# Performance work log

Measured on AMD Instinct MI355X. Metric: run time of the kernel, lower is better.

## Reference

```python
import jax, jax.numpy as jnp
import numpy as np
import itertools

B, NM, NS, K, HID, NLAYER, MAXZ, OUT = 64, 32, 32, 3, 64, 4, 100, 1
S = B * NS
NREAL = NM - 2  # real nodes per graph (rest padded)


def setup_inputs() -> dict:
    key = jax.random.key(0)
    ks = jax.random.split(key, 12)
    x = jax.random.randint(ks[0], (B, NM, 1), 0, MAXZ + 1, dtype=jnp.int32)
    subadj = jax.random.uniform(ks[1], (B, NM, NM), dtype=jnp.float32)
    # K distinct node ids per subgraph, all within the real (non-padded) nodes
    subgs = jnp.argsort(jax.random.uniform(ks[2], (S, NREAL)), axis=1)[:, :K].astype(jnp.int32)
    num_node = jnp.full((B,), NREAL, dtype=jnp.int32)
    num_subg = jnp.full((B,), NS, dtype=jnp.int32)
    sc = 0.05
    idemb = jax.random.normal(ks[3], (K + 2, HID), jnp.float32) * sc
    node_emb = jax.random.normal(ks[4], (MAXZ + 1, HID), jnp.float32) * sc
    mlp_W1 = jax.random.normal(ks[5], (NLAYER, HID, HID), jnp.float32) * sc
    mlp_b1 = jnp.zeros((NLAYER, HID), jnp.float32)
    mlp_W2 = jax.random.normal(ks[6], (NLAYER, HID, HID), jnp.float32) * sc
    mlp_b2 = jnp.zeros((NLAYER, HID), jnp.float32)
    mlp_g = jnp.ones((NLAYER, HID), jnp.float32)
    mlp_be = jnp.zeros((NLAYER, HID), jnp.float32)
    set1_W = jax.random.normal(ks[7], (HID, HID), jnp.float32) * sc
    set1_b = jnp.zeros((HID,), jnp.float32)
    set2_W = jax.random.normal(ks[8], (HID, HID), jnp.float32) * sc
    set2_b = jnp.zeros((HID,), jnp.float32)
    out_W = jax.random.normal(ks[9], (HID, OUT), jnp.float32) * sc
    out_b = jnp.zeros((OUT,), jnp.float32)
    return dict(x=x, subadj=subadj, subgs=subgs, num_node=num_node, num_subg=num_subg,
                idemb=idemb, node_emb=node_emb, mlp_W1=mlp_W1, mlp_b1=mlp_b1,
                mlp_W2=mlp_W2, mlp_b2=mlp_b2, mlp_g=mlp_g, mlp_be=mlp_be,
                set1_W=set1_W, set1_b=set1_b, set2_W=set2_W, set2_b=set2_b,
                out_W=out_W, out_b=out_b)


def _layernorm(z, g, b):
    m = z.mean(-1, keepdims=True)
    v = ((z - m) ** 2).mean(-1, keepdims=True)
    return (z - m) / jnp.sqrt(v + 1e-5) * g + b


def _forward(x, subadj, subgs, num_node,
             idemb, node_emb, mlp_W1, mlp_b1, mlp_W2, mlp_b2, mlp_g, mlp_be,
             set1_W, set1_b, set2_W, set2_b, out_W, out_b):
    # allperm: (K, K!) -- matches registered buffer extracttuple(arange(k),k).t()
    allperm = jnp.asarray(np.array(list(itertools.permutations(range(K))), dtype=np.int32).T)
    P = allperm.shape[1]  # K! permutations
    subgbatch = jnp.repeat(jnp.arange(B), NS)                       # (S,) graph id of each subgraph
    null_mask = jnp.arange(NM)[None, :] >= num_node[:, None]        # (B, NM) padded-node mask
    h = node_emb[x[..., 0]]                                         # (B, NM, HID) inmlp embedding
    h = jnp.broadcast_to(h[subgbatch][:, :, None, :], (S, NM, P, HID))  # gather per subgraph, expand perms
    # CSR scatter-assign of permutation id embeddings (all rows full size K, distinct nodes)
    labelbatch = jnp.repeat(jnp.arange(S), K)                       # (S*K,)
    labelnodes = subgs.reshape(-1)                                  # (S*K,)
    nodeidx = jnp.tile(jnp.arange(K), S)                            # position within subgraph
    emb = idemb[allperm[nodeidx]]                                   # (S*K, P, HID)
    h = h.at[labelbatch, labelnodes].multiply(emb)                  # unique (subg,node) pairs
    A = subadj[subgbatch]                                           # (S, NM, NM), float path (d=1 broadcast)
    for l in range(NLAYER):
        m = jnp.einsum('bij,bjpd->bipd', A, h)                      # noindexbmm
        m = jax.nn.relu(m @ mlp_W1[l] + mlp_b1[l])
        m = m @ mlp_W2[l] + mlp_b2[l]
        m = jax.nn.relu(_layernorm(m, mlp_g[l], mlp_be[l]))
        h = h + m
    h = jnp.where(null_mask[subgbatch][:, :, None, None], 0.0, h)   # zero padded nodes
    h = jax.nn.relu(h.mean(axis=2) @ set1_W + set1_b)               # setmlp1 over perm-mean: (S, NM, HID)
    h = jax.nn.relu(h.sum(axis=1) @ set2_W + set2_b)                # setmlp2 over node-sum: (S, HID)
    pooled = jax.ops.segment_max(h, subgbatch, num_segments=B)      # global_max_pool: (B, HID)
    return pooled @ out_W + out_b                                   # (B, OUT)


def reference(x, subadj, subgs, num_node, num_subg,
              idemb, node_emb, mlp_W1, mlp_b1, mlp_W2, mlp_b2, mlp_g, mlp_be,
              set1_W, set1_b, set2_W, set2_b, out_W, out_b):
    return _forward(x, subadj, subgs, num_node,
                    idemb, node_emb, mlp_W1, mlp_b1, mlp_W2, mlp_b2, mlp_g, mlp_be,
                    set1_W, set1_b, set2_W, set2_b, out_W, out_b)
```

## Files before the change

kernel.cpp:

```cpp
#include <hip/hip_runtime.h>
#include <math.h>


#define NBATCH 64
#define NM 32
#define NS 32
#define KSUB 3
#define HID 64
#define NLAYER 4
#define PP 6
#define STOT (NBATCH * NS)

#define W1F 0
#define W2F 16384
#define S1F 32768
#define GMAX_BYTE 73728
#define CNT_BYTE  90112
#define S2WT_BYTE 90368

#define SH 68
#define SG 36
#define WBU 2304

typedef _Float16 f16x8 __attribute__((ext_vector_type(8)));
typedef float f32x4 __attribute__((ext_vector_type(4)));

#define MFMA16(a, b, c) __builtin_amdgcn_mfma_f32_16x16x32_f16(a, b, c, 0, 0, 0)

__constant__ int c_perm[KSUB][PP] = {
    {0, 0, 1, 1, 2, 2},
    {1, 2, 0, 2, 0, 1},
    {2, 1, 2, 0, 1, 0}
};

__device__ __forceinline__ uint2 pk4(float a, float b, float c, float d) {
    union { _Float16 h[4]; uint2 u; } x;
    x.h[0] = (_Float16)a; x.h[1] = (_Float16)b;
    x.h[2] = (_Float16)c; x.h[3] = (_Float16)d;
    return x.u;
}
__device__ __forceinline__ float2 upk2(unsigned u) {
    union { unsigned u; _Float16 h[2]; } x; x.u = u;
    return make_float2((float)x.h[0], (float)x.h[1]);
}
__device__ __forceinline__ f16x8 frd(const unsigned short* p) {
    union { struct { uint2 a, b; } u; f16x8 f; } x;
    x.u.a = *(const uint2*)p;
    x.u.b = *(const uint2*)(p + 4);
    return x.f;
}
__device__ __forceinline__ f16x8 gfrd(const unsigned short* p) {
    union { uint4 u; f16x8 f; } x;
    x.u = *(const uint4*)p;
    return x.f;
}

extern "C" __global__ void idmpnn_prep(const float* __restrict__ w1,
                                       const float* __restrict__ w2,
                                       const float* __restrict__ s1w,
                                       const float* __restrict__ s2w,
                                       char* __restrict__ ws)
{
    unsigned short* wsu = (unsigned short*)ws;
    int idx = blockIdx.x * 256 + threadIdx.x;
    float v; int dst;
    if (idx < 16384) {
        int l = idx >> 12, r = idx & 4095, dp = r >> 6, e = r & 63;
        v = w1[l * 4096 + e * 64 + dp];
        dst = W1F + idx;
    } else if (idx < 32768) {
        int k = idx - 16384;
        int l = k >> 12, r = k & 4095, dp = r >> 6, e = r & 63;
        v = w2[l * 4096 + e * 64 + dp];
        dst = W2F + k;
    } else if (idx < 36864) {
        int k = idx - 32768, dp = k >> 6, e = k & 63;
        v = s1w[e * 64 + dp];
        dst = S1F + k;
    } else if (idx < 40960) {
        int k = idx - 36864, dp = k >> 6, e = k & 63;
        ((float*)(ws + S2WT_BYTE))[k] = s2w[e * 64 + dp];
        return;
    } else if (idx < 45056) {
        ((unsigned*)(ws + GMAX_BYTE))[idx - 40960] = 0u;
        return;
    } else if (idx < 45120) {
        ((unsigned*)(ws + CNT_BYTE))[idx - 45056] = 0u;
        return;
    } else return;
    union { _Float16 h; unsigned short u; } cv;
    cv.h = (_Float16)v;
    wsu[dst] = cv.u;
}

extern "C" __global__ void __launch_bounds__(384, 3)
idmpnn_main(const int* __restrict__ xg, const float* __restrict__ subadj,
            const int* __restrict__ subgs, const int* __restrict__ num_node,
            const float* __restrict__ idemb, const float* __restrict__ node_emb,
            const float* __restrict__ b1g, const float* __restrict__ b2g,
            const float* __restrict__ lngm, const float* __restrict__ lnbm,
            const float* __restrict__ s1bm, const float* __restrict__ s2bm,
            const float* __restrict__ outw, const float* __restrict__ outb,
            const unsigned short* __restrict__ wsf, const float* __restrict__ s2wt,
            unsigned* __restrict__ gmax, unsigned* __restrict__ cnt,
            float* __restrict__ out)
{
    __shared__ unsigned short WB[6 * WBU];
    __shared__ float idS[KSUB * 64];
    __shared__ float prm[NLAYER * 4 * 64];
    __shared__ float HSf[HID];

    const int s = blockIdx.x, b = s >> 5;
    const int tid = threadIdx.x;
    const int w = tid / 64, lane = tid & 63;
    const int c = lane & 15, q = lane >> 4;

    for (int t = tid; t < NLAYER * 4 * 64; t += 384) {
        int l = t >> 8, r2 = t & 255, set = r2 >> 6, d = r2 & 63;
        const float* src = (set == 0) ? b1g : (set == 1) ? b2g : (set == 2) ? lngm : lnbm;
        prm[t] = src[l * HID + d];
    }
    if (tid < KSUB * 64) idS[tid] = idemb[tid];

    const int nd0 = subgs[s * KSUB + 0];
    const int nd1 = subgs[s * KSUB + 1];
    const int nd2 = subgs[s * KSUB + 2];
    const int nn = num_node[b];
    const int zi0 = xg[b * NM + c];
    const int zi1 = xg[b * NM + 16 + c];

    f16x8 adjf[2];
#pragma unroll
    for (int in_ = 0; in_ < 2; ++in_) {
        const float* ap = subadj + (size_t)b * NM * NM + (in_ * 16 + c) * NM + 8 * q;
        float4 f0 = *(const float4*)ap;
        float4 f1 = *(const float4*)(ap + 4);
        f16x8 r;
        r[0] = (_Float16)f0.x; r[1] = (_Float16)f0.y;
        r[2] = (_Float16)f0.z; r[3] = (_Float16)f0.w;
        r[4] = (_Float16)f1.x; r[5] = (_Float16)f1.y;
        r[6] = (_Float16)f1.z; r[7] = (_Float16)f1.w;
        adjf[in_] = r;
    }

    __syncthreads();

    unsigned short* wb = WB + w * WBU;
    const int p = w;

    unsigned hpk[16];
#pragma unroll
    for (int in_ = 0; in_ < 2; ++in_) {
        int i = in_ * 16 + c;
        int z = in_ ? zi1 : zi0;
        int pid = (i == nd0) ? c_perm[0][p] : (i == nd1) ? c_perm[1][p]
                  : (i == nd2) ? c_perm[2][p] : -1;
#pragma unroll
        for (int dm = 0; dm < 4; ++dm) {
            float4 e4 = *(const float4*)(node_emb + (size_t)z * HID + dm * 16 + 4 * q);
            if (pid >= 0) {
                float4 f4 = *(const float4*)&idS[pid * 64 + dm * 16 + 4 * q];
                e4.x *= f4.x; e4.y *= f4.y; e4.z *= f4.z; e4.w *= f4.w;
            }
            uint2 u = pk4(e4.x, e4.y, e4.z, e4.w);
            hpk[in_ * 8 + dm * 2 + 0] = u.x;
            hpk[in_ * 8 + dm * 2 + 1] = u.y;
        }
    }

#pragma unroll 1
    for (int l = 0; l < NLAYER; ++l) {
#pragma unroll
        for (int in_ = 0; in_ < 2; ++in_)
#pragma unroll
            for (int dm = 0; dm < 4; ++dm)
                *(uint2*)(wb + (in_ * 16 + c) * SH + dm * 16 + 4 * q) =
                    make_uint2(hpk[in_ * 8 + dm * 2], hpk[in_ * 8 + dm * 2 + 1]);

        f16x8 hah[2][2];
#pragma unroll
        for (int im = 0; im < 2; ++im)
#pragma unroll
            for (int ks = 0; ks < 2; ++ks)
                hah[im][ks] = frd(wb + (im * 16 + c) * SH + ks * 32 + 8 * q);

#pragma unroll
        for (int jn = 0; jn < 4; ++jn) {
            const unsigned short* wp = wsf + W1F + (l * 64 + jn * 16 + c) * 64;
            f16x8 b0 = gfrd(wp + 8 * q);
            f16x8 b1 = gfrd(wp + 32 + 8 * q);
            f32x4 g0 = {0.f, 0.f, 0.f, 0.f}, g1 = {0.f, 0.f, 0.f, 0.f};
            g0 = MFMA16(hah[0][0], b0, g0);
            g0 = MFMA16(hah[0][1], b1, g0);
            g1 = MFMA16(hah[1][0], b0, g1);
            g1 = MFMA16(hah[1][1], b1, g1);
            *(uint2*)(wb + (jn * 16 + c) * SG + 4 * q)      = pk4(g0[0], g0[1], g0[2], g0[3]);
            *(uint2*)(wb + (jn * 16 + c) * SG + 16 + 4 * q) = pk4(g1[0], g1[1], g1[2], g1[3]);
        }

        f16x8 gah[4];
#pragma unroll
        for (int dm = 0; dm < 4; ++dm)
            gah[dm] = frd(wb + (dm * 16 + c) * SG + 8 * q);

#pragma unroll
        for (int dm = 0; dm < 4; ++dm) {
            float4 b1v = *(const float4*)&prm[(l * 4 + 0) * 64 + dm * 16 + 4 * q];
            f32x4 t0 = {0.f, 0.f, 0.f, 0.f}, t1 = {0.f, 0.f, 0.f, 0.f};
            t0 = MFMA16(gah[dm], adjf[0], t0);
            t1 = MFMA16(gah[dm], adjf[1], t1);
            *(uint2*)(wb + c * SH + dm * 16 + 4 * q) =
                pk4(fmaxf(t0[0] + b1v.x, 0.f), fmaxf(t0[1] + b1v.y, 0.f),
                    fmaxf(t0[2] + b1v.z, 0.f), fmaxf(t0[3] + b1v.w, 0.f));
            *(uint2*)(wb + (16 + c) * SH + dm * 16 + 4 * q) =
                pk4(fmaxf(t1[0] + b1v.x, 0.f), fmaxf(t1[1] + b1v.y, 0.f),
                    fmaxf(t1[2] + b1v.z, 0.f), fmaxf(t1[3] + b1v.w, 0.f));
        }

        f16x8 tbh[2][2];
#pragma unroll
        for (int in_ = 0; in_ < 2; ++in_)
#pragma unroll
            for (int ks = 0; ks < 2; ++ks)
                tbh[in_][ks] = frd(wb + (in_ * 16 + c) * SH + ks * 32 + 8 * q);

#pragma unroll
        for (int in_ = 0; in_ < 2; ++in_) {
            float v[16];
            float s1 = 0.f, s2 = 0.f;
#pragma unroll
            for (int dm = 0; dm < 4; ++dm) {
                const unsigned short* wp2 = wsf + W2F + (l * 64 + dm * 16 + c) * 64;
                f16x8 a0 = gfrd(wp2 + 8 * q);
                f16x8 a1 = gfrd(wp2 + 32 + 8 * q);
                f32x4 u = {0.f, 0.f, 0.f, 0.f};
                u = MFMA16(a0, tbh[in_][0], u);
                u = MFMA16(a1, tbh[in_][1], u);
                float4 b2v = *(const float4*)&prm[(l * 4 + 1) * 64 + dm * 16 + 4 * q];
                const float* bb = (const float*)&b2v;
#pragma unroll
                for (int r = 0; r < 4; ++r) {
                    float x = u[r] + bb[r];
                    v[dm * 4 + r] = x;
                    s1 += x;
                    s2 += x * x;
                }
            }
            s1 += __shfl_xor(s1, 16, 64); s1 += __shfl_xor(s1, 32, 64);
            s2 += __shfl_xor(s2, 16, 64); s2 += __shfl_xor(s2, 32, 64);
            float mean = s1 * (1.0f / HID);
            float var  = s2 * (1.0f / HID) - mean * mean;
            float rs   = rsqrtf(var + 1e-5f);
#pragma unroll
            for (int dm = 0; dm < 4; ++dm) {
                float4 gv4  = *(const float4*)&prm[(l * 4 + 2) * 64 + dm * 16 + 4 * q];
                float4 bev4 = *(const float4*)&prm[(l * 4 + 3) * 64 + dm * 16 + 4 * q];
                const float* gp = (const float*)&gv4;
                const float* bp = (const float*)&bev4;
                float y0 = fmaxf((v[dm * 4 + 0] - mean) * rs * gp[0] + bp[0], 0.f);
                float y1 = fmaxf((v[dm * 4 + 1] - mean) * rs * gp[1] + bp[1], 0.f);
                float y2 = fmaxf((v[dm * 4 + 2] - mean) * rs * gp[2] + bp[2], 0.f);
                float y3 = fmaxf((v[dm * 4 + 3] - mean) * rs * gp[3] + bp[3], 0.f);
                float2 h0 = upk2(hpk[in_ * 8 + dm * 2 + 0]);
                float2 h1 = upk2(hpk[in_ * 8 + dm * 2 + 1]);
                uint2 nu = pk4(h0.x + y0, h0.y + y1, h1.x + y2, h1.y + y3);
                hpk[in_ * 8 + dm * 2 + 0] = nu.x;
                hpk[in_ * 8 + dm * 2 + 1] = nu.y;
            }
        }
    }

#pragma unroll
    for (int in_ = 0; in_ < 2; ++in_)
#pragma unroll
        for (int dm = 0; dm < 4; ++dm)
            *(uint2*)(wb + (in_ * 16 + c) * SH + dm * 16 + 4 * q) =
                make_uint2(hpk[in_ * 8 + dm * 2], hpk[in_ * 8 + dm * 2 + 1]);
    __syncthreads();

    if (w == 0) {
        f16x8 mah[2][2];
#pragma unroll
        for (int im = 0; im < 2; ++im) {
            float sc = ((im * 16 + c) < nn) ? (1.0f / PP) : 0.f;
#pragma unroll
            for (int ks = 0; ks < 2; ++ks) {
                int ro = (im * 16 + c) * SH + ks * 32 + 8 * q;
                float acc8[8];
#pragma unroll
                for (int j = 0; j < 8; ++j) acc8[j] = 0.f;
#pragma unroll
                for (int wv = 0; wv < 6; ++wv) {
                    f16x8 f = frd(WB + wv * WBU + ro);
#pragma unroll
                    for (int j = 0; j < 8; ++j) acc8[j] += (float)f[j];
                }
                f16x8 m;
#pragma unroll
                for (int j = 0; j < 8; ++j) m[j] = (_Float16)(acc8[j] * sc);
                mah[im][ks] = m;
            }
        }

        f32x4 hh[2][4];
#pragma unroll
        for (int im = 0; im < 2; ++im)
#pragma unroll
            for (int jn = 0; jn < 4; ++jn) hh[im][jn] = (f32x4){0.f, 0.f, 0.f, 0.f};
#pragma unroll
        for (int jn = 0; jn < 4; ++jn) {
            const unsigned short* sp = wsf + S1F + (jn * 16 + c) * 64;
            f16x8 b0 = gfrd(sp + 8 * q);
            f16x8 b1 = gfrd(sp + 32 + 8 * q);
#pragma unroll
            for (int im = 0; im < 2; ++im) {
                hh[im][jn] = MFMA16(mah[im][0], b0, hh[im][jn]);
                hh[im][jn] = MFMA16(mah[im][1], b1, hh[im][jn]);
            }
        }
#pragma unroll
        for (int jn = 0; jn < 4; ++jn) {
            float sb = s1bm[jn * 16 + c];
            float cs = 0.f;
#pragma unroll
            for (int im = 0; im < 2; ++im)
#pragma unroll
                for (int r = 0; r < 4; ++r)
                    cs += fmaxf(hh[im][jn][r] + sb, 0.f);
            cs += __shfl_xor(cs, 16, 64);
            cs += __shfl_xor(cs, 32, 64);
            if (q == 0) HSf[jn * 16 + c] = cs;
        }

        float acc = 0.f;
#pragma unroll
        for (int e4 = 0; e4 < 16; ++e4) {
            float4 wv = *(const float4*)&s2wt[lane * 64 + e4 * 4];
            float4 hv = *(const float4*)&HSf[e4 * 4];
            acc += hv.x * wv.x + hv.y * wv.y + hv.z * wv.z + hv.w * wv.w;
        }
        float h2 = fmaxf(acc + s2bm[lane], 0.f);

        atomicMax(&gmax[b * HID + lane], __float_as_uint(h2));
        __threadfence();
        unsigned old = 0;
        if (lane == 0) old = atomicAdd(&cnt[b], 1u);
        old = __shfl(old, 0, 64);
        if (old == NS - 1) {
            __threadfence();
            unsigned mbits = atomicOr(&gmax[b * HID + lane], 0u);
            float v = __uint_as_float(mbits) * outw[lane];
#pragma unroll
            for (int off = 32; off > 0; off >>= 1) v += __shfl_xor(v, off, 64);
            if (lane == 0) out[b] = v + outb[0];
        }
    }
}

extern "C" void kernel_launch(void* const* d_in, const int* in_sizes, int n_in,
                              void* d_out, int out_size, void* d_ws, size_t ws_size,
                              hipStream_t stream)
{
    const int*   xg       = (const int*)d_in[0];
    const float* subadj   = (const float*)d_in[1];
    const int*   subgs    = (const int*)d_in[2];
    const int*   num_node = (const int*)d_in[3];
    const float* idemb    = (const float*)d_in[5];
    const float* node_emb = (const float*)d_in[6];
    const float* w1       = (const float*)d_in[7];
    const float* b1       = (const float*)d_in[8];
    const float* w2       = (const float*)d_in[9];
    const float* b2       = (const float*)d_in[10];
    const float* g        = (const float*)d_in[11];
    const float* be       = (const float*)d_in[12];
    const float* s1w      = (const float*)d_in[13];
    const float* s1b      = (const float*)d_in[14];
    const float* s2w      = (const float*)d_in[15];
    const float* s2b      = (const float*)d_in[16];
    const float* outw     = (const float*)d_in[17];
    const float* outb     = (const float*)d_in[18];

    char* ws = (char*)d_ws;
    unsigned short* wsf = (unsigned short*)ws;
    const float* s2wt = (const float*)(ws + S2WT_BYTE);
    unsigned* gmax = (unsigned*)(ws + GMAX_BYTE);
    unsigned* cnt  = (unsigned*)(ws + CNT_BYTE);

    idmpnn_prep<<<177, 256, 0, stream>>>(w1, w2, s1w, s2w, ws);
    idmpnn_main<<<STOT, 384, 0, stream>>>(xg, subadj, subgs, num_node, idemb, node_emb,
                                          b1, b2, g, be, s1b, s2b, outw, outb,
                                          wsf, s2wt, gmax, cnt, (float*)d_out);
}
```

Baseline: 249.9 us.

## Process two subgraphs per block to share weight and adjacency loads

Each block now handles two subgraphs of the same graph, so the W1/W2 fragments loaded from global, the adjacency fragments and the per-layer parameters are reused across both, with interleaved MFMA chains for more instruction-level parallelism. Float-to-half conversions switch to the packed round-toward-zero intrinsic, and the residual add is done in packed half precision. The cost is doubled LDS and register use, with launch bounds lowered from 3 to 2 blocks per SM and half as many blocks, plus slightly different rounding.

After: 215.8 us. 1.16x faster.

```diff
diff --git a/kernel.cpp b/kernel.cpp
--- a/kernel.cpp
+++ b/kernel.cpp
@@ -9,7 +9,6 @@
 #define HID 64
 #define NLAYER 4
 #define PP 6
-#define STOT (NBATCH * NS)
 
 #define W1F 0
 #define W2F 16384
@@ -23,6 +22,8 @@
 #define WBU 2304
 
 typedef _Float16 f16x8 __attribute__((ext_vector_type(8)));
+typedef _Float16 f16x2 __attribute__((ext_vector_type(2)));
+typedef __fp16 fp16x2 __attribute__((ext_vector_type(2)));
 typedef float f32x4 __attribute__((ext_vector_type(4)));
 
 #define MFMA16(a, b, c) __builtin_amdgcn_mfma_f32_16x16x32_f16(a, b, c, 0, 0, 0)
@@ -33,15 +34,19 @@
     {2, 1, 2, 0, 1, 0}
 };
 
-__device__ __forceinline__ uint2 pk4(float a, float b, float c, float d) {
-    union { _Float16 h[4]; uint2 u; } x;
-    x.h[0] = (_Float16)a; x.h[1] = (_Float16)b;
-    x.h[2] = (_Float16)c; x.h[3] = (_Float16)d;
+__device__ __forceinline__ unsigned pk2rtz(float a, float b) {
+    union { fp16x2 h; unsigned u; } x;
+    x.h = __builtin_amdgcn_cvt_pkrtz(a, b);
     return x.u;
 }
-__device__ __forceinline__ float2 upk2(unsigned u) {
-    union { unsigned u; _Float16 h[2]; } x; x.u = u;
-    return make_float2((float)x.h[0], (float)x.h[1]);
+__device__ __forceinline__ uint2 pk4rtz(float a, float b, float c, float d) {
+    return make_uint2(pk2rtz(a, b), pk2rtz(c, d));
+}
+__device__ __forceinline__ unsigned pkadd(unsigned hu, unsigned yu) {
+    union { f16x2 h; unsigned u; } a, b;
+    a.u = hu; b.u = yu;
+    a.h = a.h + b.h;
+    return a.u;
 }
 __device__ __forceinline__ f16x8 frd(const unsigned short* p) {
     union { struct { uint2 a, b; } u; f16x8 f; } x;
@@ -93,7 +98,7 @@
     wsu[dst] = cv.u;
 }
 
-extern "C" __global__ void __launch_bounds__(384, 3)
+extern "C" __global__ void __launch_bounds__(384, 2)
 idmpnn_main(const int* __restrict__ xg, const float* __restrict__ subadj,
             const int* __restrict__ subgs, const int* __restrict__ num_node,
             const float* __restrict__ idemb, const float* __restrict__ node_emb,
@@ -105,12 +110,13 @@
             unsigned* __restrict__ gmax, unsigned* __restrict__ cnt,
             float* __restrict__ out)
 {
-    __shared__ unsigned short WB[6 * WBU];
+    __shared__ unsigned short WB[12 * WBU];
     __shared__ float idS[KSUB * 64];
     __shared__ float prm[NLAYER * 4 * 64];
-    __shared__ float HSf[HID];
-
-    const int s = blockIdx.x, b = s >> 5;
+    __shared__ float HSf[2 * HID];
+
+    const int s0 = blockIdx.x * 2;
+    const int b = s0 >> 5;
     const int tid = threadIdx.x;
     const int w = tid / 64, lane = tid & 63;
     const int c = lane & 15, q = lane >> 4;
@@ -122,9 +128,12 @@
     }
     if (tid < KSUB * 64) idS[tid] = idemb[tid];
 
-    const int nd0 = subgs[s * KSUB + 0];
-    const int nd1 = subgs[s * KSUB + 1];
-    const int nd2 = subgs[s * KSUB + 2];
+    int nd[2][3];
+#pragma unroll
+    for (int ch = 0; ch < 2; ++ch)
+#pragma unroll
+        for (int k = 0; k < 3; ++k)
+            nd[ch][k] = subgs[(s0 + ch) * KSUB + k];
     const int nn = num_node[b];
     const int zi0 = xg[b * NM + c];
     const int zi1 = xg[b * NM + 16 + c];
@@ -135,150 +144,176 @@
         const float* ap = subadj + (size_t)b * NM * NM + (in_ * 16 + c) * NM + 8 * q;
         float4 f0 = *(const float4*)ap;
         float4 f1 = *(const float4*)(ap + 4);
-        f16x8 r;
-        r[0] = (_Float16)f0.x; r[1] = (_Float16)f0.y;
-        r[2] = (_Float16)f0.z; r[3] = (_Float16)f0.w;
-        r[4] = (_Float16)f1.x; r[5] = (_Float16)f1.y;
-        r[6] = (_Float16)f1.z; r[7] = (_Float16)f1.w;
-        adjf[in_] = r;
+        union { struct { uint2 a, b; } u; f16x8 f; } x;
+        x.u.a = pk4rtz(f0.x, f0.y, f0.z, f0.w);
+        x.u.b = pk4rtz(f1.x, f1.y, f1.z, f1.w);
+        adjf[in_] = x.f;
     }
 
     __syncthreads();
 
-    unsigned short* wb = WB + w * WBU;
+    unsigned short* wbc[2] = { WB + (w * 2 + 0) * WBU, WB + (w * 2 + 1) * WBU };
     const int p = w;
 
-    unsigned hpk[16];
+    unsigned hpk[2][16];
 #pragma unroll
     for (int in_ = 0; in_ < 2; ++in_) {
         int i = in_ * 16 + c;
         int z = in_ ? zi1 : zi0;
-        int pid = (i == nd0) ? c_perm[0][p] : (i == nd1) ? c_perm[1][p]
-                  : (i == nd2) ? c_perm[2][p] : -1;
+        int pid[2];
+#pragma unroll
+        for (int ch = 0; ch < 2; ++ch)
+            pid[ch] = (i == nd[ch][0]) ? c_perm[0][p] : (i == nd[ch][1]) ? c_perm[1][p]
+                      : (i == nd[ch][2]) ? c_perm[2][p] : -1;
 #pragma unroll
         for (int dm = 0; dm < 4; ++dm) {
             float4 e4 = *(const float4*)(node_emb + (size_t)z * HID + dm * 16 + 4 * q);
-            if (pid >= 0) {
-                float4 f4 = *(const float4*)&idS[pid * 64 + dm * 16 + 4 * q];
-                e4.x *= f4.x; e4.y *= f4.y; e4.z *= f4.z; e4.w *= f4.w;
-            }
-            uint2 u = pk4(e4.x, e4.y, e4.z, e4.w);
-            hpk[in_ * 8 + dm * 2 + 0] = u.x;
-            hpk[in_ * 8 + dm * 2 + 1] = u.y;
+#pragma unroll
+            for (int ch = 0; ch < 2; ++ch) {
+                float4 v = e4;
+                if (pid[ch] >= 0) {
+                    float4 f4 = *(const float4*)&idS[pid[ch] * 64 + dm * 16 + 4 * q];
+                    v.x *= f4.x; v.y *= f4.y; v.z *= f4.z; v.w *= f4.w;
+                }
+                uint2 u = pk4rtz(v.x, v.y, v.z, v.w);
+                hpk[ch][in_ * 8 + dm * 2 + 0] = u.x;
+                hpk[ch][in_ * 8 + dm * 2 + 1] = u.y;
+            }
         }
     }
 
 #pragma unroll 1
     for (int l = 0; l < NLAYER; ++l) {
 #pragma unroll
-        for (int in_ = 0; in_ < 2; ++in_)
-#pragma unroll
-            for (int dm = 0; dm < 4; ++dm)
-                *(uint2*)(wb + (in_ * 16 + c) * SH + dm * 16 + 4 * q) =
-                    make_uint2(hpk[in_ * 8 + dm * 2], hpk[in_ * 8 + dm * 2 + 1]);
-
-        f16x8 hah[2][2];
-#pragma unroll
-        for (int im = 0; im < 2; ++im)
-#pragma unroll
-            for (int ks = 0; ks < 2; ++ks)
-                hah[im][ks] = frd(wb + (im * 16 + c) * SH + ks * 32 + 8 * q);
+        for (int ch = 0; ch < 2; ++ch)
+#pragma unroll
+            for (int in_ = 0; in_ < 2; ++in_)
+#pragma unroll
+                for (int dm = 0; dm < 4; ++dm)
+                    *(uint2*)(wbc[ch] + (in_ * 16 + c) * SH + dm * 16 + 4 * q) =
+                        make_uint2(hpk[ch][in_ * 8 + dm * 2], hpk[ch][in_ * 8 + dm * 2 + 1]);
+
+        f16x8 hah[2][2][2];
+#pragma unroll
+        for (int ch = 0; ch < 2; ++ch)
+#pragma unroll
+            for (int im = 0; im < 2; ++im)
+#pragma unroll
+                for (int ks = 0; ks < 2; ++ks)
+                    hah[ch][im][ks] = frd(wbc[ch] + (im * 16 + c) * SH + ks * 32 + 8 * q);
 
 #pragma unroll
         for (int jn = 0; jn < 4; ++jn) {
             const unsigned short* wp = wsf + W1F + (l * 64 + jn * 16 + c) * 64;
             f16x8 b0 = gfrd(wp + 8 * q);
             f16x8 b1 = gfrd(wp + 32 + 8 * q);
-            f32x4 g0 = {0.f, 0.f, 0.f, 0.f}, g1 = {0.f, 0.f, 0.f, 0.f};
-            g0 = MFMA16(hah[0][0], b0, g0);
-            g0 = MFMA16(hah[0][1], b1, g0);
-            g1 = MFMA16(hah[1][0], b0, g1);
-            g1 = MFMA16(hah[1][1], b1, g1);
-            *(uint2*)(wb + (jn * 16 + c) * SG + 4 * q)      = pk4(g0[0], g0[1], g0[2], g0[3]);
-            *(uint2*)(wb + (jn * 16 + c) * SG + 16 + 4 * q) = pk4(g1[0], g1[1], g1[2], g1[3]);
-        }
-
-        f16x8 gah[4];
-#pragma unroll
-        for (int dm = 0; dm < 4; ++dm)
-            gah[dm] = frd(wb + (dm * 16 + c) * SG + 8 * q);
+#pragma unroll
+            for (int ch = 0; ch < 2; ++ch) {
+                f32x4 g0 = {0.f, 0.f, 0.f, 0.f}, g1 = {0.f, 0.f, 0.f, 0.f};
+                g0 = MFMA16(hah[ch][0][0], b0, g0);
+                g0 = MFMA16(hah[ch][0][1], b1, g0);
+                g1 = MFMA16(hah[ch][1][0], b0, g1);
+                g1 = MFMA16(hah[ch][1][1], b1, g1);
+                *(uint2*)(wbc[ch] + (jn * 16 + c) * SG + 4 * q)      = pk4rtz(g0[0], g0[1], g0[2], g0[3]);
+                *(uint2*)(wbc[ch] + (jn * 16 + c) * SG + 16 + 4 * q) = pk4rtz(g1[0], g1[1], g1[2], g1[3]);
+            }
+        }
+
+        f16x8 gah[2][4];
+#pragma unroll
+        for (int ch = 0; ch < 2; ++ch)
+#pragma unroll
+            for (int dm = 0; dm < 4; ++dm)
+                gah[ch][dm] = frd(wbc[ch] + (dm * 16 + c) * SG + 8 * q);
 
 #pragma unroll
         for (int dm = 0; dm < 4; ++dm) {
             float4 b1v = *(const float4*)&prm[(l * 4 + 0) * 64 + dm * 16 + 4 * q];
-            f32x4 t0 = {0.f, 0.f, 0.f, 0.f}, t1 = {0.f, 0.f, 0.f, 0.f};
-            t0 = MFMA16(gah[dm], adjf[0], t0);
-            t1 = MFMA16(gah[dm], adjf[1], t1);
-            *(uint2*)(wb + c * SH + dm * 16 + 4 * q) =
-                pk4(fmaxf(t0[0] + b1v.x, 0.f), fmaxf(t0[1] + b1v.y, 0.f),
-                    fmaxf(t0[2] + b1v.z, 0.f), fmaxf(t0[3] + b1v.w, 0.f));
-            *(uint2*)(wb + (16 + c) * SH + dm * 16 + 4 * q) =
-                pk4(fmaxf(t1[0] + b1v.x, 0.f), fmaxf(t1[1] + b1v.y, 0.f),
-                    fmaxf(t1[2] + b1v.z, 0.f), fmaxf(t1[3] + b1v.w, 0.f));
-        }
-
-        f16x8 tbh[2][2];
-#pragma unroll
-        for (int in_ = 0; in_ < 2; ++in_)
-#pragma unroll
-            for (int ks = 0; ks < 2; ++ks)
-                tbh[in_][ks] = frd(wb + (in_ * 16 + c) * SH + ks * 32 + 8 * q);
+#pragma unroll
+            for (int ch = 0; ch < 2; ++ch) {
+                f32x4 t0 = {0.f, 0.f, 0.f, 0.f}, t1 = {0.f, 0.f, 0.f, 0.f};
+                t0 = MFMA16(gah[ch][dm], adjf[0], t0);
+                t1 = MFMA16(gah[ch][dm], adjf[1], t1);
+                *(uint2*)(wbc[ch] + c * SH + dm * 16 + 4 * q) =
+                    pk4rtz(fmaxf(t0[0] + b1v.x, 0.f), fmaxf(t0[1] + b1v.y, 0.f),
+                           fmaxf(t0[2] + b1v.z, 0.f), fmaxf(t0[3] + b1v.w, 0.f));
+                *(uint2*)(wbc[ch] + (16 + c) * SH + dm * 16 + 4 * q) =
+                    pk4rtz(fmaxf(t1[0] + b1v.x, 0.f), fmaxf(t1[1] + b1v.y, 0.f),
+                           fmaxf(t1[2] + b1v.z, 0.f), fmaxf(t1[3] + b1v.w, 0.f));
+            }
+        }
+
+        f16x8 tbh[2][2][2];
+#pragma unroll
+        for (int ch = 0; ch < 2; ++ch)
+#pragma unroll
+            for (int in_ = 0; in_ < 2; ++in_)
+#pragma unroll
+                for (int ks = 0; ks < 2; ++ks)
+                    tbh[ch][in_][ks] = frd(wbc[ch] + (in_ * 16 + c) * SH + ks * 32 + 8 * q);
 
 #pragma unroll
         for (int in_ = 0; in_ < 2; ++in_) {
-            float v[16];
-            float s1 = 0.f, s2 = 0.f;
+            float v[2][16];
+            float s1[2] = {0.f, 0.f}, s2[2] = {0.f, 0.f};
 #pragma unroll
             for (int dm = 0; dm < 4; ++dm) {
                 const unsigned short* wp2 = wsf + W2F + (l * 64 + dm * 16 + c) * 64;
                 f16x8 a0 = gfrd(wp2 + 8 * q);
                 f16x8 a1 = gfrd(wp2 + 32 + 8 * q);
-                f32x4 u = {0.f, 0.f, 0.f, 0.f};
-                u = MFMA16(a0, tbh[in_][0], u);
-                u = MFMA16(a1, tbh[in_][1], u);
                 float4 b2v = *(const float4*)&prm[(l * 4 + 1) * 64 + dm * 16 + 4 * q];
                 const float* bb = (const float*)&b2v;
 #pragma unroll
-                for (int r = 0; r < 4; ++r) {
-                    float x = u[r] + bb[r];
-                    v[dm * 4 + r] = x;
-                    s1 += x;
-                    s2 += x * x;
+                for (int ch = 0; ch < 2; ++ch) {
+                    f32x4 u = {0.f, 0.f, 0.f, 0.f};
+                    u = MFMA16(a0, tbh[ch][in_][0], u);
+                    u = MFMA16(a1, tbh[ch][in_][1], u);
+#pragma unroll
+                    for (int r = 0; r < 4; ++r) {
+                        float x = u[r] + bb[r];
+                        v[ch][dm * 4 + r] = x;
+                        s1[ch] += x;
+                        s2[ch] += x * x;
+                    }
                 }
             }
-            s1 += __shfl_xor(s1, 16, 64); s1 += __shfl_xor(s1, 32, 64);
-            s2 += __shfl_xor(s2, 16, 64); s2 += __shfl_xor(s2, 32, 64);
-            float mean = s1 * (1.0f / HID);
-            float var  = s2 * (1.0f / HID) - mean * mean;
-            float rs   = rsqrtf(var + 1e-5f);
-#pragma unroll
-            for (int dm = 0; dm < 4; ++dm) {
-                float4 gv4  = *(const float4*)&prm[(l * 4 + 2) * 64 + dm * 16 + 4 * q];
-                float4 bev4 = *(const float4*)&prm[(l * 4 + 3) * 64 + dm * 16 + 4 * q];
-                const float* gp = (const float*)&gv4;
-                const float* bp = (const float*)&bev4;
-                float y0 = fmaxf((v[dm * 4 + 0] - mean) * rs * gp[0] + bp[0], 0.f);
-                float y1 = fmaxf((v[dm * 4 + 1] - mean) * rs * gp[1] + bp[1], 0.f);
-                float y2 = fmaxf((v[dm * 4 + 2] - mean) * rs * gp[2] + bp[2], 0.f);
-                float y3 = fmaxf((v[dm * 4 + 3] - mean) * rs * gp[3] + bp[3], 0.f);
-                float2 h0 = upk2(hpk[in_ * 8 + dm * 2 + 0]);
-                float2 h1 = upk2(hpk[in_ * 8 + dm * 2 + 1]);
-                uint2 nu = pk4(h0.x + y0, h0.y + y1, h1.x + y2, h1.y + y3);
-                hpk[in_ * 8 + dm * 2 + 0] = nu.x;
-                hpk[in_ * 8 + dm * 2 + 1] = nu.y;
+#pragma unroll
+            for (int ch = 0; ch < 2; ++ch) {
+                float a1 = s1[ch], a2 = s2[ch];
+                a1 += __shfl_xor(a1, 16, 64); a1 += __shfl_xor(a1, 32, 64);
+                a2 += __shfl_xor(a2, 16, 64); a2 += __shfl_xor(a2, 32, 64);
+                float mean = a1 * (1.0f / HID);
+                float var  = a2 * (1.0f / HID) - mean * mean;
+                float rs   = rsqrtf(var + 1e-5f);
+#pragma unroll
+                for (int dm = 0; dm < 4; ++dm) {
+                    float4 gv4  = *(const float4*)&prm[(l * 4 + 2) * 64 + dm * 16 + 4 * q];
+                    float4 bev4 = *(const float4*)&prm[(l * 4 + 3) * 64 + dm * 16 + 4 * q];
+                    const float* gp = (const float*)&gv4;
+                    const float* bp = (const float*)&bev4;
+                    float y0 = fmaxf((v[ch][dm * 4 + 0] - mean) * rs * gp[0] + bp[0], 0.f);
+                    float y1 = fmaxf((v[ch][dm * 4 + 1] - mean) * rs * gp[1] + bp[1], 0.f);
+                    float y2 = fmaxf((v[ch][dm * 4 + 2] - mean) * rs * gp[2] + bp[2], 0.f);
+                    float y3 = fmaxf((v[ch][dm * 4 + 3] - mean) * rs * gp[3] + bp[3], 0.f);
+                    int i0 = in_ * 8 + dm * 2;
+                    hpk[ch][i0 + 0] = pkadd(hpk[ch][i0 + 0], pk2rtz(y0, y1));
+                    hpk[ch][i0 + 1] = pkadd(hpk[ch][i0 + 1], pk2rtz(y2, y3));
+                }
             }
         }
     }
 
 #pragma unroll
-    for (int in_ = 0; in_ < 2; ++in_)
-#pragma unroll
-        for (int dm = 0; dm < 4; ++dm)
-            *(uint2*)(wb + (in_ * 16 + c) * SH + dm * 16 + 4 * q) =
-                make_uint2(hpk[in_ * 8 + dm * 2], hpk[in_ * 8 + dm * 2 + 1]);
+    for (int ch = 0; ch < 2; ++ch)
+#pragma unroll
+        for (int in_ = 0; in_ < 2; ++in_)
+#pragma unroll
+            for (int dm = 0; dm < 4; ++dm)
+                *(uint2*)(wbc[ch] + (in_ * 16 + c) * SH + dm * 16 + 4 * q) =
+                    make_uint2(hpk[ch][in_ * 8 + dm * 2], hpk[ch][in_ * 8 + dm * 2 + 1]);
     __syncthreads();
 
-    if (w == 0) {
+    if (w < 2) {
         f16x8 mah[2][2];
 #pragma unroll
         for (int im = 0; im < 2; ++im) {
@@ -291,7 +326,7 @@
                 for (int j = 0; j < 8; ++j) acc8[j] = 0.f;
 #pragma unroll
                 for (int wv = 0; wv < 6; ++wv) {
-                    f16x8 f = frd(WB + wv * WBU + ro);
+                    f16x8 f = frd(WB + (wv * 2 + w) * WBU + ro);
 #pragma unroll
                     for (int j = 0; j < 8; ++j) acc8[j] += (float)f[j];
                 }
@@ -329,14 +364,14 @@
                     cs += fmaxf(hh[im][jn][r] + sb, 0.f);
             cs += __shfl_xor(cs, 16, 64);
             cs += __shfl_xor(cs, 32, 64);
-            if (q == 0) HSf[jn * 16 + c] = cs;
+            if (q == 0) HSf[w * HID + jn * 16 + c] = cs;
         }
 
         float acc = 0.f;
 #pragma unroll
         for (int e4 = 0; e4 < 16; ++e4) {
             float4 wv = *(const float4*)&s2wt[lane * 64 + e4 * 4];
-            float4 hv = *(const float4*)&HSf[e4 * 4];
+            float4 hv = *(const float4*)&HSf[w * HID + e4 * 4];
             acc += hv.x * wv.x + hv.y * wv.y + hv.z * wv.z + hv.w * wv.w;
         }
         float h2 = fmaxf(acc + s2bm[lane], 0.f);
@@ -387,7 +422,8 @@
     unsigned* cnt  = (unsigned*)(ws + CNT_BYTE);
 
     idmpnn_prep<<<177, 256, 0, stream>>>(w1, w2, s1w, s2w, ws);
-    idmpnn_main<<<STOT, 384, 0, stream>>>(xg, subadj, subgs, num_node, idemb, node_emb,
+    idmpnn_main<<<NBATCH * NS / 2, 384, 0, stream>>>(xg, subadj, subgs, num_node,
+                                          idemb, node_emb,
                                           b1, b2, g, be, s1b, s2b, outw, outb,
                                           wsf, s2wt, gmax, cnt, (float*)d_out);
 }
```
